# Optimization experiments

Hardware: AMD Instinct MI355X
Metric: run time of the kernel (lower is better)

Reference implementation:

```python
import jax, jax.numpy as jnp
import numpy as np

B, T, H = 1024, 128, 256
EPS = 1e-5


def _lstm(x, W_ih, W_hh, b_ih, b_hh):
    # x: [B,T,D] -> hs: [B,T,H], hn: [B,H]; PyTorch gate order i,f,g,o
    xp = jnp.einsum('btd,gd->btg', x, W_ih) + b_ih + b_hh  # [B,T,4H]
    h0 = jnp.zeros((x.shape[0], W_hh.shape[1]), x.dtype)

    def step(carry, xt):
        h, c = carry
        g = xt + h @ W_hh.T
        i, f, gg, o = jnp.split(g, 4, axis=-1)
        c = jax.nn.sigmoid(f) * c + jax.nn.sigmoid(i) * jnp.tanh(gg)
        h = jax.nn.sigmoid(o) * jnp.tanh(c)
        return (h, c), h

    (hn, _), hs = jax.lax.scan(step, (h0, h0), jnp.swapaxes(xp, 0, 1))
    return jnp.swapaxes(hs, 0, 1), hn


def _bn(x, g, b, m, v):
    # eval-mode BatchNorm1d
    return g * (x - m) * jax.lax.rsqrt(v + EPS) + b


def setup_inputs() -> dict:
    key = jax.random.key(0)
    ks = jax.random.split(key, 40)
    f = lambda i, shape, s=0.05: jax.random.normal(ks[i], shape, jnp.float32) * s
    d = {}
    d['seq_cont_data'] = f(0, (B, T, 64), 1.0)
    d['seq_cat_data'] = jax.random.randint(ks[1], (B, T, 2), 0, 500)
    d['non_seq_cat_data'] = jax.random.randint(ks[2], (B, 2), 0, 1000)
    d['non_seq_cont_data'] = f(3, (B, 32), 1.0)
    d['emb_ns0'] = f(4, (10000, 64))
    d['emb_ns1'] = f(5, (1000, 64))
    d['emb_s0'] = f(6, (1000, 32))
    d['emb_s1'] = f(7, (500, 32))
    d['W_ih'] = f(8, (4 * H, 128)); d['W_hh'] = f(9, (4 * H, H))
    d['b_ih'] = f(10, (4 * H,)); d['b_hh'] = f(11, (4 * H,))
    d['W_ltd'] = f(12, (H, H)); d['b_ltd'] = f(13, (H,))
    d['W_conv'] = f(14, (H, T)); d['b_conv'] = f(15, (H,))
    d['W_tpa'] = f(16, (H, H)); d['W_tpa_h'] = f(17, (H, H)); d['W_tpa_c'] = f(18, (H, H))
    FIN = 672
    d['W_f1'] = f(19, (512, FIN)); d['b_f1'] = f(20, (512,))
    d['g1'] = 1.0 + f(21, (512,)); d['be1'] = f(22, (512,)); d['m1'] = f(23, (512,)); d['v1'] = jnp.ones((512,), jnp.float32)
    d['W_f2'] = f(24, (256, 512)); d['b_f2'] = f(25, (256,))
    d['g2'] = 1.0 + f(26, (256,)); d['be2'] = f(27, (256,)); d['m2'] = f(28, (256,)); d['v2'] = jnp.ones((256,), jnp.float32)
    d['W_out'] = f(29, (64, 256)); d['b_out'] = f(30, (64,))
    return d


def reference(seq_cont_data, seq_cat_data, non_seq_cat_data, non_seq_cont_data,
              emb_ns0, emb_ns1, emb_s0, emb_s1,
              W_ih, W_hh, b_ih, b_hh, W_ltd, b_ltd, W_conv, b_conv,
              W_tpa, W_tpa_h, W_tpa_c,
              W_f1, b_f1, g1, be1, m1, v1,
              W_f2, b_f2, g2, be2, m2, v2,
              W_out, b_out):
    # non-sequential input: embeddings + continuous
    ns_cat = jnp.concatenate([emb_ns0[non_seq_cat_data[:, 0]], emb_ns1[non_seq_cat_data[:, 1]]], axis=1)
    non_seq_inp = jnp.concatenate([ns_cat, non_seq_cont_data], axis=1)  # [B,160]
    # sequential input: embeddings + continuous
    s_cat = jnp.concatenate([emb_s0[seq_cat_data[:, :, 0]], emb_s1[seq_cat_data[:, :, 1]]], axis=2)
    seq_data = jnp.concatenate([s_cat, seq_cont_data], axis=2)  # [B,T,128]
    output, hn = _lstm(seq_data, W_ih, W_hh, b_ih, b_hh)  # [B,T,H], [B,H]
    # TPA: hc[b,i,j] = Conv1d_j(output[:,:,i]) = sum_t output[b,t,i]*W_conv[j,t] + b_conv[j]
    hc = jnp.einsum('bti,jt->bij', output, W_conv) + b_conv  # [B,H,H]
    # alpha[b,i] = sigmoid( (hc[b,i] @ W_tpa.T) . hn[b] )
    alpha = jax.nn.sigmoid(jnp.einsum('bik,bk->bi', jnp.einsum('bij,kj->bik', hc, W_tpa), hn))
    vt = jnp.einsum('bi,bih->bh', alpha, hc)  # [B,H]
    htprime = hn @ W_tpa_h.T + vt @ W_tpa_c.T
    seq_inp = hn @ W_ltd.T + b_ltd
    fin_input = jnp.concatenate([non_seq_inp, seq_inp, htprime], axis=1)  # [B,672]
    x = _bn(jax.nn.relu(fin_input @ W_f1.T + b_f1), g1, be1, m1, v1)
    x = _bn(jax.nn.relu(x @ W_f2.T + b_f2), g2, be2, m2, v2)
    x = jax.nn.relu(x @ W_out.T + b_out)
    return x, fin_input
```

## Files before the change

kernel.cpp:

```cpp
#include <hip/hip_runtime.h>
#include <hip/hip_bf16.h>
#include <math.h>

#define B_SZ 1024
#define T_SZ 128
#define H_SZ 256
#define DIN  128
#define G4   1024
#define FINW 672

using bf16   = __hip_bfloat16;
using short8 = __attribute__((ext_vector_type(8))) short;
using f32x4  = __attribute__((ext_vector_type(4))) float;

__device__ __forceinline__ float bf2f(bf16 x) { return __bfloat162float(x); }
__device__ __forceinline__ bf16  f2bf(float x) { return __float2bfloat16(x); }
__device__ __forceinline__ float sigm(float x) { return 1.0f / (1.0f + __expf(-x)); }
__device__ __forceinline__ float ftanh(float x) { return 2.0f / (1.0f + __expf(-2.0f * x)) - 1.0f; }
__device__ __forceinline__ float bfraw2f(unsigned short r) {
  unsigned u = ((unsigned)r) << 16;
  return *reinterpret_cast<float*>(&u);
}

struct Ptrs { const void* p[33]; };

#define NSEG 30
__device__ __host__ constexpr int kSegOffArr(int i) {
  constexpr int off[NSEG + 1] = {
      0,       32768,   672768,  736768,  768768,  784768,  915840,
      1177984, 1179008, 1180032, 1245568, 1245824, 1278592, 1278848,
      1344384, 1409920, 1475456, 1819520, 1820032, 1820544, 1821056,
      1821568, 1822080, 1953152, 1953408, 1953664, 1953920, 1954176,
      1954432, 1970816, 1970880};
  return off[i];
}
#define ARENA_TOTAL 1970880
#define TR_BASE   1970880
#define TR_WthT   0
#define TR_WtcT   65536
#define TR_WltT   131072
#define TR_WcvT   196608
#define TR_TOTAL  229376
#define ARENA_TOTAL2 (ARENA_TOTAL + TR_TOTAL)

__global__ __launch_bounds__(256) void k_convert(Ptrs pk, bf16* __restrict__ dst,
                                                 uint4* __restrict__ hsp) {
  bool isf32 = ((((const unsigned*)pk.p[24])[0] & 0xFFFFu) == 0u);
  int stride = gridDim.x * blockDim.x;
  int gtid = blockIdx.x * blockDim.x + threadIdx.x;
  for (int i = gtid; i < ARENA_TOTAL; i += stride) {
    int s = 0, base = 0;
#pragma unroll
    for (int j = 1; j < NSEG; j++) {
      bool ge = (i >= kSegOffArr(j));
      s    = ge ? j : s;
      base = ge ? kSegOffArr(j) : base;
    }
    int off = i - base;
    const void* src = pk.p[3 + s];
    dst[i] = isf32 ? f2bf(((const float*)src)[off]) : ((const bf16*)src)[off];
  }
  for (int j = gtid; j < TR_TOTAL; j += stride) {
    const void* src;
    int off;
    if (j < TR_WtcT)      { src = pk.p[17]; int jj = j;            off = (jj & 255) * 256 + (jj >> 8); }
    else if (j < TR_WltT) { src = pk.p[18]; int jj = j - TR_WtcT;  off = (jj & 255) * 256 + (jj >> 8); }
    else if (j < TR_WcvT) { src = pk.p[12]; int jj = j - TR_WltT;  off = (jj & 255) * 256 + (jj >> 8); }
    else                  { src = pk.p[14]; int jj = j - TR_WcvT;  off = (jj & 255) * 128 + (jj >> 8); }
    dst[TR_BASE + j] = isf32 ? f2bf(((const float*)src)[off]) : ((const bf16*)src)[off];
  }
  uint4 pv = make_uint4(0xFFFFFFFFu, 0xFFFFFFFFu, 0xFFFFFFFFu, 0xFFFFFFFFu);
  for (int i = gtid; i < (int)((size_t)T_SZ * B_SZ * H_SZ * 2 / 16); i += stride)
    hsp[i] = pv;
}

__global__ __launch_bounds__(256) void k_gather(
    const void* __restrict__ seq_cont_raw, const int* __restrict__ seq_cat,
    const bf16* __restrict__ emb_s0, const bf16* __restrict__ emb_s1,
    bf16* __restrict__ seq_out, const unsigned* __restrict__ probe) {
  bool isf32 = ((probe[0] & 0xFFFFu) == 0u);
  int gid = blockIdx.x * blockDim.x + threadIdx.x;
  int seg = gid & 15;
  int m   = gid >> 4;
  int t   = m >> 10;
  int b   = m & 1023;
  bf16* dst = seq_out + (long)m * DIN + seg * 8;
  if (seg < 8) {
    const bf16* src;
    if (seg < 4) {
      int idx = seq_cat[(b * T_SZ + t) * 2 + 0];
      src = emb_s0 + idx * 32 + seg * 8;
    } else {
      int idx = seq_cat[(b * T_SZ + t) * 2 + 1];
      src = emb_s1 + idx * 32 + (seg - 4) * 8;
    }
    *reinterpret_cast<short8*>(dst) = *reinterpret_cast<const short8*>(src);
  } else {
    long base = ((long)b * T_SZ + t) * 64 + (seg - 8) * 8;
    if (isf32) {
      const float4* sp =
          reinterpret_cast<const float4*>((const float*)seq_cont_raw + base);
      float4 x0 = sp[0], x1 = sp[1];
      union { short8 v; bf16 h[8]; } u;
      u.h[0] = f2bf(x0.x); u.h[1] = f2bf(x0.y); u.h[2] = f2bf(x0.z); u.h[3] = f2bf(x0.w);
      u.h[4] = f2bf(x1.x); u.h[5] = f2bf(x1.y); u.h[6] = f2bf(x1.z); u.h[7] = f2bf(x1.w);
      *reinterpret_cast<short8*>(dst) = u.v;
    } else {
      *reinterpret_cast<short8*>(dst) =
          *reinterpret_cast<const short8*>((const bf16*)seq_cont_raw + base);
    }
  }
}

#define HPOISON 0xFFFFFFFFu
__global__ __launch_bounds__(512, 2) void k_lstm(
    const bf16* __restrict__ seq, const bf16* __restrict__ Wih,
    const bf16* __restrict__ Whh, const bf16* __restrict__ bih,
    const bf16* __restrict__ bhh, bf16* __restrict__ hs) {
  __shared__ short8 hsh[2][8 * 64];
  __shared__ short8 xsh[2][4 * 64];
  int tid  = threadIdx.x;
  int w    = tid >> 6, lane = tid & 63;
  int quad = lane >> 4, l15 = lane & 15;
  int bid  = blockIdx.x;
  int gid  = bid & 63;
  int rank = bid >> 6;
  int peer = 1 - rank;
  long b0  = (long)gid * 16;
  int hup = w * 16 + l15;
  int hu  = rank * 128 + hup;

  { short8 z = {0,0,0,0,0,0,0,0}; hsh[0][tid] = z; }

  float bia[4];
#pragma unroll
  for (int i = 0; i < 4; ++i) {
    int grow = i * H_SZ + hu;
    bia[i] = bf2f(bih[grow]) + bf2f(bhh[grow]);
  }

  short8 wif[4][4];
  short8 whfS[4][4];
  short8 whfP[4][4];
#pragma unroll
  for (int i = 0; i < 4; ++i) {
    long grow = (long)(i * H_SZ + rank * 128 + hup);
#pragma unroll
    for (int kt = 0; kt < 4; ++kt) {
      wif[i][kt] = *reinterpret_cast<const short8*>(
          Wih + grow * DIN + kt * 32 + quad * 8);
      whfS[i][kt] = *reinterpret_cast<const short8*>(
          Whh + grow * H_SZ + (rank * 4 + kt) * 32 + quad * 8);
      whfP[i][kt] = *reinterpret_cast<const short8*>(
          Whh + grow * H_SZ + (peer * 4 + kt) * 32 + quad * 8);
    }
  }
  if (tid < 256)
    xsh[0][tid] = *reinterpret_cast<const short8*>(
        seq + (b0 + (tid & 15)) * DIN + (tid >> 6) * 32 +
        ((tid >> 4) & 3) * 8);
  float c[4] = {0.f, 0.f, 0.f, 0.f};
  __syncthreads();

  for (int t = 0; t < T_SZ; ++t) {
    int cur = t & 1, nxt = cur ^ 1;
    short8 xpre;
    bool dopre = (t + 1 < T_SZ) & (tid < 256);
    if (dopre)
      xpre = *reinterpret_cast<const short8*>(
          seq + ((long)(t + 1) * B_SZ + b0 + (tid & 15)) * DIN +
          (tid >> 6) * 32 + ((tid >> 4) & 3) * 8);

    f32x4 acc[4];
#pragma unroll
    for (int i = 0; i < 4; ++i) acc[i] = {0.f, 0.f, 0.f, 0.f};

#pragma unroll
    for (int kt = 0; kt < 4; ++kt) {
      short8 ax = xsh[cur][kt * 64 + lane];
#pragma unroll
      for (int i = 0; i < 4; ++i)
        acc[i] = __builtin_amdgcn_mfma_f32_16x16x32_bf16(ax, wif[i][kt], acc[i], 0, 0, 0);
    }
#pragma unroll
    for (int kt = 0; kt < 4; ++kt) {
      short8 ah = hsh[cur][(rank * 4 + kt) * 64 + lane];
#pragma unroll
      for (int i = 0; i < 4; ++i)
        acc[i] = __builtin_amdgcn_mfma_f32_16x16x32_bf16(ah, whfS[i][kt], acc[i], 0, 0, 0);
    }

    if (t > 0) {
      if (tid < 256) {
        int m = tid >> 4, seg = tid & 15;
        const unsigned* src = reinterpret_cast<const unsigned*>(
            hs + ((long)(t - 1) * B_SZ + b0 + m) * H_SZ + peer * 128 + seg * 8);
        unsigned d0, d1, d2, d3;
        do {
          d0 = __hip_atomic_load(src + 0, __ATOMIC_RELAXED, __HIP_MEMORY_SCOPE_AGENT);
          d1 = __hip_atomic_load(src + 1, __ATOMIC_RELAXED, __HIP_MEMORY_SCOPE_AGENT);
          d2 = __hip_atomic_load(src + 2, __ATOMIC_RELAXED, __HIP_MEMORY_SCOPE_AGENT);
          d3 = __hip_atomic_load(src + 3, __ATOMIC_RELAXED, __HIP_MEMORY_SCOPE_AGENT);
        } while (d0 == HPOISON || d1 == HPOISON || d2 == HPOISON || d3 == HPOISON);
        union { unsigned u[4]; short8 s; } cv;
        cv.u[0] = d0; cv.u[1] = d1; cv.u[2] = d2; cv.u[3] = d3;
        hsh[cur][(peer * 4 + (seg >> 2)) * 64 + (seg & 3) * 16 + m] = cv.s;
      }
      __syncthreads();
    }
#pragma unroll
    for (int kt = 0; kt < 4; ++kt) {
      short8 ah = hsh[cur][(peer * 4 + kt) * 64 + lane];
#pragma unroll
      for (int i = 0; i < 4; ++i)
        acc[i] = __builtin_amdgcn_mfma_f32_16x16x32_bf16(ah, whfP[i][kt], acc[i], 0, 0, 0);
    }

    bf16* hbn = reinterpret_cast<bf16*>(&hsh[nxt][0]);
    unsigned hpk[4];
#pragma unroll
    for (int r = 0; r < 4; ++r) {
      float iv = sigm(acc[0][r] + bia[0]);
      float fv = sigm(acc[1][r] + bia[1]);
      float gv = ftanh(acc[2][r] + bia[2]);
      float ov = sigm(acc[3][r] + bia[3]);
      c[r] = fv * c[r] + iv * gv;
      bf16 hv = f2bf(ov * ftanh(c[r]));
      int m = quad * 4 + r;
      hbn[(((hu >> 5) * 64) + ((hu >> 3) & 3) * 16 + m) * 8 + (hu & 7)] = hv;
      unsigned hraw = (unsigned)*reinterpret_cast<unsigned short*>(&hv);
      unsigned nb = (unsigned)__shfl_down((int)hraw, 1, 64);
      hpk[r] = hraw | (nb << 16);
    }
    if (dopre) xsh[nxt][tid] = xpre;
    __syncthreads();
    if ((l15 & 1) == 0) {
#pragma unroll
      for (int r = 0; r < 4; ++r) {
        int m = quad * 4 + r;
        unsigned* dst = reinterpret_cast<unsigned*>(
            hs + ((long)t * B_SZ + b0 + m) * H_SZ + hu);
        __hip_atomic_store(dst, hpk[r], __ATOMIC_RELAXED,
                           __HIP_MEMORY_SCOPE_AGENT);
      }
    }
  }
}

__global__ __launch_bounds__(256) void k_u(
    const bf16* __restrict__ hs, const bf16* __restrict__ W_tpa,
    const bf16* __restrict__ W_conv, const bf16* __restrict__ b_conv,
    float* __restrict__ w2, float* __restrict__ c0) {
  __shared__ float hn_sh[8][256];
  __shared__ float u_sh[8][256];
  __shared__ float wred[4][8];
  int tid = threadIdx.x;
  long b0 = (long)blockIdx.x * 8;
#pragma unroll
  for (int r = 0; r < 8; r++)
    hn_sh[r][tid] = bf2f(hs[((long)(T_SZ - 1) * B_SZ + b0 + r) * H_SZ + tid]);
  __syncthreads();
  float u[8] = {0,0,0,0,0,0,0,0};
  for (int kk = 0; kk < 32; kk++) {
    float wv[8];
#pragma unroll
    for (int q = 0; q < 8; q++)
      wv[q] = bf2f(W_tpa[(kk * 8 + q) * H_SZ + tid]);
#pragma unroll
    for (int r = 0; r < 8; r++) {
      const float4* hp = reinterpret_cast<const float4*>(&hn_sh[r][kk * 8]);
      float4 h0 = hp[0], h1 = hp[1];
      u[r] += h0.x * wv[0]; u[r] += h0.y * wv[1];
      u[r] += h0.z * wv[2]; u[r] += h0.w * wv[3];
      u[r] += h1.x * wv[4]; u[r] += h1.y * wv[5];
      u[r] += h1.z * wv[6]; u[r] += h1.w * wv[7];
    }
  }
  float bc = bf2f(b_conv[tid]);
  float p[8];
#pragma unroll
  for (int r = 0; r < 8; r++) { u_sh[r][tid] = u[r]; p[r] = u[r] * bc; }
#pragma unroll
  for (int d = 32; d > 0; d >>= 1)
#pragma unroll
    for (int r = 0; r < 8; r++) p[r] += __shfl_down(p[r], d, 64);
  if ((tid & 63) == 0)
#pragma unroll
    for (int r = 0; r < 8; r++) wred[tid >> 6][r] = p[r];
  __syncthreads();
  if (tid < 8)
    c0[b0 + tid] = wred[0][tid] + wred[1][tid] + wred[2][tid] + wred[3][tid];
  if (tid < T_SZ) {
    float a[8] = {0,0,0,0,0,0,0,0};
    for (int jj = 0; jj < 32; jj++) {
      float wv[8];
#pragma unroll
      for (int q = 0; q < 8; q++)
        wv[q] = bf2f(W_conv[(jj * 8 + q) * T_SZ + tid]);
#pragma unroll
      for (int r = 0; r < 8; r++) {
        const float4* up = reinterpret_cast<const float4*>(&u_sh[r][jj * 8]);
        float4 u0 = up[0], u1 = up[1];
        a[r] += u0.x * wv[0]; a[r] += u0.y * wv[1];
        a[r] += u0.z * wv[2]; a[r] += u0.w * wv[3];
        a[r] += u1.x * wv[4]; a[r] += u1.y * wv[5];
        a[r] += u1.z * wv[6]; a[r] += u1.w * wv[7];
      }
    }
#pragma unroll
    for (int r = 0; r < 8; r++) w2[(b0 + r) * T_SZ + tid] = a[r];
  }
}

__global__ __launch_bounds__(256) void k_alphas(
    const bf16* __restrict__ hs, const float* __restrict__ w2,
    const float* __restrict__ c0, float* __restrict__ asum,
    float* __restrict__ sbuf) {
  __shared__ unsigned hc[128 * 129];
  __shared__ float w2s[T_SZ];
  __shared__ float ash[H_SZ];
  __shared__ float red[256];
  int b = blockIdx.x, tid = threadIdx.x;
#pragma unroll
  for (int p = 0; p < 16; p++) {
    int task = p * 256 + tid;
    int row = task >> 5, seg = task & 31;
    short8 v = *reinterpret_cast<const short8*>(
        hs + ((long)row * B_SZ + b) * H_SZ + seg * 8);
    union { short8 s; unsigned u[4]; } cv; cv.s = v;
#pragma unroll
    for (int k = 0; k < 4; k++) hc[row * 129 + seg * 4 + k] = cv.u[k];
  }
  if (tid < T_SZ) w2s[tid] = w2[b * T_SZ + tid];
  __syncthreads();
  {
    float ap = c0[b];
    int wi = tid >> 1, hi = tid & 1;
    for (int t = 0; t < T_SZ; t++) {
      unsigned uv = hc[t * 129 + wi];
      unsigned short h16 = hi ? (unsigned short)(uv >> 16) : (unsigned short)(uv & 0xFFFF);
      float hvf = __bfloat162float(*reinterpret_cast<bf16*>(&h16));
      ap += hvf * w2s[t];
    }
    float a = sigm(ap);
    ash[tid] = a;
    red[tid] = a;
  }
  __syncthreads();
  for (int s = 128; s > 0; s >>= 1) {
    if (tid < s) red[tid] += red[tid + s];
    __syncthreads();
  }
  if (tid == 0) asum[b] = red[0];
  if (tid < T_SZ) {
    float acc = 0.f;
    for (int k = 0; k < 128; k++) {
      int wi = (k + tid) & 127;
      unsigned uv = hc[tid * 129 + wi];
      unsigned short lo16 = (unsigned short)(uv & 0xFFFF);
      unsigned short hi16 = (unsigned short)(uv >> 16);
      float lo = __bfloat162float(*reinterpret_cast<bf16*>(&lo16));
      float hi = __bfloat162float(*reinterpret_cast<bf16*>(&hi16));
      acc += ash[2 * wi] * lo + ash[2 * wi + 1] * hi;
    }
    sbuf[b * T_SZ + tid] = acc;
  }
}

__global__ __launch_bounds__(256) void k_fin(
    const bf16* __restrict__ hs, const float* __restrict__ sbuf,
    const float* __restrict__ asum, const bf16* __restrict__ WcvT,
    const bf16* __restrict__ b_conv, const bf16* __restrict__ WthT,
    const bf16* __restrict__ WtcT, const bf16* __restrict__ WltT,
    const bf16* __restrict__ b_ltd, const int* __restrict__ ns_cat,
    const bf16* __restrict__ emb_ns0, const bf16* __restrict__ emb_ns1,
    const bf16* __restrict__ ns_cont, float* __restrict__ fin,
    void* __restrict__ d_out_raw, const unsigned* __restrict__ probe) {
  bool isf32 = ((probe[0] & 0xFFFFu) == 0u);
  __shared__ float s_sh[8][128];
  __shared__ float hn_sh[8][256];
  __shared__ float vt_sh[8][256];
  int tid = threadIdx.x;
  long b0 = (long)blockIdx.x * 8;
  auto store2 = [&](int r, int pos, float v) {
    fin[(b0 + r) * FINW + pos] = v;
    if (isf32)
      ((float*)d_out_raw + 65536)[(b0 + r) * FINW + pos] = v;
    else
      ((bf16*)d_out_raw + 65536)[(b0 + r) * FINW + pos] = f2bf(v);
  };
  if (tid < 128)
#pragma unroll
    for (int r = 0; r < 8; r++) s_sh[r][tid] = sbuf[(b0 + r) * T_SZ + tid];
#pragma unroll
  for (int r = 0; r < 8; r++)
    hn_sh[r][tid] = bf2f(hs[((long)(T_SZ - 1) * B_SZ + b0 + r) * H_SZ + tid]);
  __syncthreads();
  float vt[8] = {0,0,0,0,0,0,0,0};
  for (int tt = 0; tt < 16; tt++) {
    float wv[8];
#pragma unroll
    for (int q = 0; q < 8; q++)
      wv[q] = bf2f(WcvT[(tt * 8 + q) * H_SZ + tid]);
#pragma unroll
    for (int r = 0; r < 8; r++) {
      const float4* sp = reinterpret_cast<const float4*>(&s_sh[r][tt * 8]);
      float4 s0 = sp[0], s1 = sp[1];
      vt[r] += wv[0] * s0.x; vt[r] += wv[1] * s0.y;
      vt[r] += wv[2] * s0.z; vt[r] += wv[3] * s0.w;
      vt[r] += wv[4] * s1.x; vt[r] += wv[5] * s1.y;
      vt[r] += wv[6] * s1.z; vt[r] += wv[7] * s1.w;
    }
  }
  float bc = bf2f(b_conv[tid]);
#pragma unroll
  for (int r = 0; r < 8; r++) {
    vt[r] += bc * asum[b0 + r];
    vt_sh[r][tid] = vt[r];
  }
  __syncthreads();
  float htp[8] = {0,0,0,0,0,0,0,0}, sq[8] = {0,0,0,0,0,0,0,0};
  for (int kk = 0; kk < 32; kk++) {
    float wh[8], wc[8], wl[8];
#pragma unroll
    for (int q = 0; q < 8; q++) {
      int k = kk * 8 + q;
      wh[q] = bf2f(WthT[k * H_SZ + tid]);
      wc[q] = bf2f(WtcT[k * H_SZ + tid]);
      wl[q] = bf2f(WltT[k * H_SZ + tid]);
    }
#pragma unroll
    for (int r = 0; r < 8; r++) {
      const float4* hp = reinterpret_cast<const float4*>(&hn_sh[r][kk * 8]);
      const float4* vp = reinterpret_cast<const float4*>(&vt_sh[r][kk * 8]);
      float4 h0 = hp[0], h1 = hp[1], v0 = vp[0], v1 = vp[1];
      htp[r] += h0.x * wh[0] + v0.x * wc[0]; sq[r] += h0.x * wl[0];
      htp[r] += h0.y * wh[1] + v0.y * wc[1]; sq[r] += h0.y * wl[1];
      htp[r] += h0.z * wh[2] + v0.z * wc[2]; sq[r] += h0.z * wl[2];
      htp[r] += h0.w * wh[3] + v0.w * wc[3]; sq[r] += h0.w * wl[3];
      htp[r] += h1.x * wh[4] + v1.x * wc[4]; sq[r] += h1.x * wl[4];
      htp[r] += h1.y * wh[5] + v1.y * wc[5]; sq[r] += h1.y * wl[5];
      htp[r] += h1.z * wh[6] + v1.z * wc[6]; sq[r] += h1.z * wl[6];
      htp[r] += h1.w * wh[7] + v1.w * wc[7]; sq[r] += h1.w * wl[7];
    }
  }
  float bl = bf2f(b_ltd[tid]);
#pragma unroll
  for (int r = 0; r < 8; r++) {
    store2(r, 160 + tid, sq[r] + bl);
    store2(r, 416 + tid, htp[r]);
  }
  if (tid < 160) {
#pragma unroll
    for (int r = 0; r < 8; r++) {
      long b = b0 + r;
      float v;
      if (tid < 64)       v = bf2f(emb_ns0[(long)ns_cat[b * 2 + 0] * 64 + tid]);
      else if (tid < 128) v = bf2f(emb_ns1[(long)ns_cat[b * 2 + 1] * 64 + tid - 64]);
      else                v = bf2f(ns_cont[b * 32 + tid - 128]);
      store2(r, tid, v);
    }
  }
}

using short4v = __attribute__((ext_vector_type(4))) short;
__global__ __launch_bounds__(512) void k_mlp(
    const float* __restrict__ fin, const bf16* __restrict__ W_f1,
    const bf16* __restrict__ b_f1, const bf16* __restrict__ g1,
    const bf16* __restrict__ be1, const bf16* __restrict__ m1,
    const bf16* __restrict__ v1, const bf16* __restrict__ W_f2,
    const bf16* __restrict__ b_f2, const bf16* __restrict__ g2,
    const bf16* __restrict__ be2, const bf16* __restrict__ m2,
    const bf16* __restrict__ v2, const bf16* __restrict__ W_out,
    const bf16* __restrict__ b_out, void* __restrict__ d_out_raw,
    const unsigned* __restrict__ probe) {
  bool isf32 = ((probe[0] & 0xFFFFu) == 0u);
  __shared__ float a_sh[FINW * 8];
  __shared__ float x1t[512 * 8];
  __shared__ float x2t[256 * 8];
  int tid = threadIdx.x;
  long b0 = (long)blockIdx.x * 8;
  for (int i = tid; i < 8 * FINW; i += 512) {
    int r = i / FINW, k = i - r * FINW;
    a_sh[k * 8 + r] = fin[b0 * FINW + i];
  }
  __syncthreads();
  {
    int n = tid;
    float acc[8] = {0, 0, 0, 0, 0, 0, 0, 0};
    const short4v* wr4 = reinterpret_cast<const short4v*>(W_f1 + (long)n * FINW);
    for (int kk = 0; kk < FINW / 4; kk++) {
      short4v w4 = wr4[kk];
#pragma unroll
      for (int j = 0; j < 4; j++) {
        float wv = bfraw2f((unsigned short)w4[j]);
        const float4* ap = reinterpret_cast<const float4*>(&a_sh[(kk * 4 + j) * 8]);
        float4 a0 = ap[0], a1 = ap[1];
        acc[0] += wv * a0.x; acc[1] += wv * a0.y;
        acc[2] += wv * a0.z; acc[3] += wv * a0.w;
        acc[4] += wv * a1.x; acc[5] += wv * a1.y;
        acc[6] += wv * a1.z; acc[7] += wv * a1.w;
      }
    }
    float bb = bf2f(b_f1[n]);
    float scale = bf2f(g1[n]) * rsqrtf(bf2f(v1[n]) + 1e-5f);
    float mm = bf2f(m1[n]), bee = bf2f(be1[n]);
#pragma unroll
    for (int r = 0; r < 8; r++) {
      float x = acc[r] + bb;
      x = x > 0.f ? x : 0.f;
      x1t[n * 8 + r] = (x - mm) * scale + bee;
    }
  }
  __syncthreads();
  if (tid < 256) {
    int n = tid;
    float acc[8] = {0, 0, 0, 0, 0, 0, 0, 0};
    const short8* wr8 = reinterpret_cast<const short8*>(W_f2 + (long)n * 512);
    for (int kk = 0; kk < 64; kk++) {
      short8 w8 = wr8[kk];
#pragma unroll
      for (int j = 0; j < 8; j++) {
        float wv = bfraw2f((unsigned short)w8[j]);
        const float4* ap = reinterpret_cast<const float4*>(&x1t[(kk * 8 + j) * 8]);
        float4 a0 = ap[0], a1 = ap[1];
        acc[0] += wv * a0.x; acc[1] += wv * a0.y;
        acc[2] += wv * a0.z; acc[3] += wv * a0.w;
        acc[4] += wv * a1.x; acc[5] += wv * a1.y;
        acc[6] += wv * a1.z; acc[7] += wv * a1.w;
      }
    }
    float bb = bf2f(b_f2[n]);
    float scale = bf2f(g2[n]) * rsqrtf(bf2f(v2[n]) + 1e-5f);
    float mm = bf2f(m2[n]), bee = bf2f(be2[n]);
#pragma unroll
    for (int r = 0; r < 8; r++) {
      float x = acc[r] + bb;
      x = x > 0.f ? x : 0.f;
      x2t[n * 8 + r] = (x - mm) * scale + bee;
    }
  }
  __syncthreads();
  if (tid < 64) {
    int n = tid;
    float acc[8] = {0, 0, 0, 0, 0, 0, 0, 0};
    const short8* wr8 = reinterpret_cast<const short8*>(W_out + (long)n * H_SZ);
    for (int kk = 0; kk < 32; kk++) {
      short8 w8 = wr8[kk];
#pragma unroll
      for (int j = 0; j < 8; j++) {
        float wv = bfraw2f((unsigned short)w8[j]);
        const float4* ap = reinterpret_cast<const float4*>(&x2t[(kk * 8 + j) * 8]);
        float4 a0 = ap[0], a1 = ap[1];
        acc[0] += wv * a0.x; acc[1] += wv * a0.y;
        acc[2] += wv * a0.z; acc[3] += wv * a0.w;
        acc[4] += wv * a1.x; acc[5] += wv * a1.y;
        acc[6] += wv * a1.z; acc[7] += wv * a1.w;
      }
    }
    float bb = bf2f(b_out[n]);
#pragma unroll
    for (int r = 0; r < 8; r++) {
      float x = acc[r] + bb;
      x = x > 0.f ? x : 0.f;
      if (isf32)
        ((float*)d_out_raw)[(b0 + r) * 64 + n] = x;
      else
        ((bf16*)d_out_raw)[(b0 + r) * 64 + n] = f2bf(x);
    }
  }
}

extern "C" void kernel_launch(void* const* d_in, const int* in_sizes, int n_in,
                              void* d_out, int out_size, void* d_ws,
                              size_t ws_size, hipStream_t stream) {
  const int* seq_cat = (const int*)d_in[1];
  const int* ns_cat  = (const int*)d_in[2];
  const unsigned* probe = (const unsigned*)d_in[24];

  char* ws = (char*)d_ws;
  bf16* seqd  = (bf16*)ws;  ws += (size_t)T_SZ * B_SZ * DIN * 2;
  bf16* hsb   = (bf16*)ws;  ws += (size_t)T_SZ * B_SZ * H_SZ * 2;
  bf16* arena = (bf16*)ws;  ws += (size_t)ARENA_TOTAL2 * 2;
  float* w2   = (float*)ws; ws += (size_t)B_SZ * T_SZ * 4;
  float* c0   = (float*)ws; ws += (size_t)B_SZ * 4;
  float* asum = (float*)ws; ws += (size_t)B_SZ * 4;
  float* sbuf = (float*)ws; ws += (size_t)B_SZ * T_SZ * 4;
  float* fin  = (float*)ws; ws += (size_t)B_SZ * FINW * 4;

  const bf16* c_ns_cont = arena + 0;
  const bf16* c_emb_ns0 = arena + 32768;
  const bf16* c_emb_ns1 = arena + 672768;
  const bf16* c_emb_s0  = arena + 736768;
  const bf16* c_emb_s1  = arena + 768768;
  const bf16* c_W_ih    = arena + 784768;
  const bf16* c_W_hh    = arena + 915840;
  const bf16* c_b_ih    = arena + 1177984;
  const bf16* c_b_hh    = arena + 1179008;
  const bf16* c_b_ltd   = arena + 1245568;
  const bf16* c_b_conv  = arena + 1278592;
  const bf16* c_W_tpa   = arena + 1278848;
  const bf16* c_W_conv  = arena + 1245824;
  const bf16* c_W_f1    = arena + 1475456;
  const bf16* c_b_f1    = arena + 1819520;
  const bf16* c_g1      = arena + 1820032;
  const bf16* c_be1     = arena + 1820544;
  const bf16* c_m1      = arena + 1821056;
  const bf16* c_v1      = arena + 1821568;
  const bf16* c_W_f2    = arena + 1822080;
  const bf16* c_b_f2    = arena + 1953152;
  const bf16* c_g2      = arena + 1953408;
  const bf16* c_be2     = arena + 1953664;
  const bf16* c_m2      = arena + 1953920;
  const bf16* c_v2      = arena + 1954176;
  const bf16* c_W_out   = arena + 1954432;
  const bf16* c_b_out   = arena + 1970816;
  const bf16* c_WthT    = arena + TR_BASE + TR_WthT;
  const bf16* c_WtcT    = arena + TR_BASE + TR_WtcT;
  const bf16* c_WltT    = arena + TR_BASE + TR_WltT;
  const bf16* c_WcvT    = arena + TR_BASE + TR_WcvT;

  Ptrs pk;
  for (int i = 0; i < 33; i++) pk.p[i] = d_in[i];

  k_convert<<<dim3(512), 256, 0, stream>>>(pk, arena, (uint4*)hsb);
  k_gather<<<dim3(B_SZ * T_SZ * 16 / 256), 256, 0, stream>>>(
      d_in[0], seq_cat, c_emb_s0, c_emb_s1, seqd, probe);
  k_lstm<<<dim3(128), 512, 0, stream>>>(seqd, c_W_ih, c_W_hh, c_b_ih, c_b_hh,
                                        hsb);
  k_u<<<dim3(B_SZ / 8), 256, 0, stream>>>(hsb, c_W_tpa, c_W_conv, c_b_conv, w2, c0);
  k_alphas<<<dim3(B_SZ), 256, 0, stream>>>(hsb, w2, c0, asum, sbuf);
  k_fin<<<dim3(B_SZ / 8), 256, 0, stream>>>(hsb, sbuf, asum, c_WcvT, c_b_conv,
                                            c_WthT, c_WtcT, c_WltT,
                                            c_b_ltd, ns_cat, c_emb_ns0,
                                            c_emb_ns1, c_ns_cont, fin, d_out,
                                            probe);
  k_mlp<<<dim3(B_SZ / 8), 512, 0, stream>>>(fin, c_W_f1, c_b_f1, c_g1, c_be1,
                                            c_m1, c_v1, c_W_f2, c_b_f2, c_g2,
                                            c_be2, c_m2, c_v2, c_W_out, c_b_out,
                                            d_out, probe);
}
```

Baseline: 682.7 us.

## Fuse embedding gather into LSTM and merge fin/MLP kernels

Removes the separate gather kernel: the LSTM now builds each input fragment on the fly from the embedding tables and continuous data, so the staged seq buffer is neither written nor re-read. It also merges the fin and MLP kernels into one 512-thread kernel that keeps fin_input in shared memory instead of sending it through a global workspace. The trade-off is that the latency-bound LSTM prefetch now does dependent index loads plus fp32 conversion inside the recurrent loop, and the merged kernel uses more shared memory.

```diff
diff --git a/kernel.cpp b/kernel.cpp
--- a/kernel.cpp
+++ b/kernel.cpp
@@ -11,6 +11,7 @@
 
 using bf16   = __hip_bfloat16;
 using short8 = __attribute__((ext_vector_type(8))) short;
+using short4v = __attribute__((ext_vector_type(4))) short;
 using f32x4  = __attribute__((ext_vector_type(4))) float;
 
 __device__ __forceinline__ float bf2f(bf16 x) { return __bfloat162float(x); }
@@ -74,51 +75,43 @@
     hsp[i] = pv;
 }
 
-__global__ __launch_bounds__(256) void k_gather(
-    const void* __restrict__ seq_cont_raw, const int* __restrict__ seq_cat,
-    const bf16* __restrict__ emb_s0, const bf16* __restrict__ emb_s1,
-    bf16* __restrict__ seq_out, const unsigned* __restrict__ probe) {
-  bool isf32 = ((probe[0] & 0xFFFFu) == 0u);
-  int gid = blockIdx.x * blockDim.x + threadIdx.x;
-  int seg = gid & 15;
-  int m   = gid >> 4;
-  int t   = m >> 10;
-  int b   = m & 1023;
-  bf16* dst = seq_out + (long)m * DIN + seg * 8;
-  if (seg < 8) {
-    const bf16* src;
-    if (seg < 4) {
-      int idx = seq_cat[(b * T_SZ + t) * 2 + 0];
-      src = emb_s0 + idx * 32 + seg * 8;
-    } else {
-      int idx = seq_cat[(b * T_SZ + t) * 2 + 1];
-      src = emb_s1 + idx * 32 + (seg - 4) * 8;
-    }
-    *reinterpret_cast<short8*>(dst) = *reinterpret_cast<const short8*>(src);
+__device__ __forceinline__ short8 x_frag(
+    const void* __restrict__ cont_raw, bool isf32,
+    const int* __restrict__ seq_cat, const bf16* __restrict__ e0,
+    const bf16* __restrict__ e1, int b, int t, int kt, int qq) {
+  int f = kt * 32 + qq * 8;
+  if (kt == 0) {
+    int idx = seq_cat[(b * T_SZ + t) * 2 + 0];
+    return *reinterpret_cast<const short8*>(e0 + idx * 32 + f);
+  } else if (kt == 1) {
+    int idx = seq_cat[(b * T_SZ + t) * 2 + 1];
+    return *reinterpret_cast<const short8*>(e1 + idx * 32 + (f - 32));
   } else {
-    long base = ((long)b * T_SZ + t) * 64 + (seg - 8) * 8;
+    long base = ((long)b * T_SZ + t) * 64 + (f - 64);
     if (isf32) {
       const float4* sp =
-          reinterpret_cast<const float4*>((const float*)seq_cont_raw + base);
+          reinterpret_cast<const float4*>((const float*)cont_raw + base);
       float4 x0 = sp[0], x1 = sp[1];
       union { short8 v; bf16 h[8]; } u;
       u.h[0] = f2bf(x0.x); u.h[1] = f2bf(x0.y); u.h[2] = f2bf(x0.z); u.h[3] = f2bf(x0.w);
       u.h[4] = f2bf(x1.x); u.h[5] = f2bf(x1.y); u.h[6] = f2bf(x1.z); u.h[7] = f2bf(x1.w);
-      *reinterpret_cast<short8*>(dst) = u.v;
+      return u.v;
     } else {
-      *reinterpret_cast<short8*>(dst) =
-          *reinterpret_cast<const short8*>((const bf16*)seq_cont_raw + base);
+      return *reinterpret_cast<const short8*>((const bf16*)cont_raw + base);
     }
   }
 }
 
 #define HPOISON 0xFFFFFFFFu
 __global__ __launch_bounds__(512, 2) void k_lstm(
-    const bf16* __restrict__ seq, const bf16* __restrict__ Wih,
-    const bf16* __restrict__ Whh, const bf16* __restrict__ bih,
-    const bf16* __restrict__ bhh, bf16* __restrict__ hs) {
+    const void* __restrict__ cont_raw, const int* __restrict__ seq_cat,
+    const bf16* __restrict__ emb_s0, const bf16* __restrict__ emb_s1,
+    const bf16* __restrict__ Wih, const bf16* __restrict__ Whh,
+    const bf16* __restrict__ bih, const bf16* __restrict__ bhh,
+    bf16* __restrict__ hs, const unsigned* __restrict__ probe) {
   __shared__ short8 hsh[2][8 * 64];
   __shared__ short8 xsh[2][4 * 64];
+  bool isf32 = ((probe[0] & 0xFFFFu) == 0u);
   int tid  = threadIdx.x;
   int w    = tid >> 6, lane = tid & 63;
   int quad = lane >> 4, l15 = lane & 15;
@@ -129,6 +122,7 @@
   long b0  = (long)gid * 16;
   int hup = w * 16 + l15;
   int hu  = rank * 128 + hup;
+  int pm = tid & 15, pkt = tid >> 6, pqq = (tid >> 4) & 3;
 
   { short8 z = {0,0,0,0,0,0,0,0}; hsh[0][tid] = z; }
 
@@ -156,9 +150,8 @@
     }
   }
   if (tid < 256)
-    xsh[0][tid] = *reinterpret_cast<const short8*>(
-        seq + (b0 + (tid & 15)) * DIN + (tid >> 6) * 32 +
-        ((tid >> 4) & 3) * 8);
+    xsh[0][tid] = x_frag(cont_raw, isf32, seq_cat, emb_s0, emb_s1,
+                         (int)(b0 + pm), 0, pkt, pqq);
   float c[4] = {0.f, 0.f, 0.f, 0.f};
   __syncthreads();
 
@@ -167,9 +160,8 @@
     short8 xpre;
     bool dopre = (t + 1 < T_SZ) & (tid < 256);
     if (dopre)
-      xpre = *reinterpret_cast<const short8*>(
-          seq + ((long)(t + 1) * B_SZ + b0 + (tid & 15)) * DIN +
-          (tid >> 6) * 32 + ((tid >> 4) & 3) * 8);
+      xpre = x_frag(cont_raw, isf32, seq_cat, emb_s0, emb_s1,
+                    (int)(b0 + pm), t + 1, pkt, pqq);
 
     f32x4 acc[4];
 #pragma unroll
@@ -367,105 +359,14 @@
   }
 }
 
-__global__ __launch_bounds__(256) void k_fin(
+__global__ __launch_bounds__(512) void k_finmlp(
     const bf16* __restrict__ hs, const float* __restrict__ sbuf,
     const float* __restrict__ asum, const bf16* __restrict__ WcvT,
     const bf16* __restrict__ b_conv, const bf16* __restrict__ WthT,
     const bf16* __restrict__ WtcT, const bf16* __restrict__ WltT,
     const bf16* __restrict__ b_ltd, const int* __restrict__ ns_cat,
     const bf16* __restrict__ emb_ns0, const bf16* __restrict__ emb_ns1,
-    const bf16* __restrict__ ns_cont, float* __restrict__ fin,
-    void* __restrict__ d_out_raw, const unsigned* __restrict__ probe) {
-  bool isf32 = ((probe[0] & 0xFFFFu) == 0u);
-  __shared__ float s_sh[8][128];
-  __shared__ float hn_sh[8][256];
-  __shared__ float vt_sh[8][256];
-  int tid = threadIdx.x;
-  long b0 = (long)blockIdx.x * 8;
-  auto store2 = [&](int r, int pos, float v) {
-    fin[(b0 + r) * FINW + pos] = v;
-    if (isf32)
-      ((float*)d_out_raw + 65536)[(b0 + r) * FINW + pos] = v;
-    else
-      ((bf16*)d_out_raw + 65536)[(b0 + r) * FINW + pos] = f2bf(v);
-  };
-  if (tid < 128)
-#pragma unroll
-    for (int r = 0; r < 8; r++) s_sh[r][tid] = sbuf[(b0 + r) * T_SZ + tid];
-#pragma unroll
-  for (int r = 0; r < 8; r++)
-    hn_sh[r][tid] = bf2f(hs[((long)(T_SZ - 1) * B_SZ + b0 + r) * H_SZ + tid]);
-  __syncthreads();
-  float vt[8] = {0,0,0,0,0,0,0,0};
-  for (int tt = 0; tt < 16; tt++) {
-    float wv[8];
-#pragma unroll
-    for (int q = 0; q < 8; q++)
-      wv[q] = bf2f(WcvT[(tt * 8 + q) * H_SZ + tid]);
-#pragma unroll
-    for (int r = 0; r < 8; r++) {
-      const float4* sp = reinterpret_cast<const float4*>(&s_sh[r][tt * 8]);
-      float4 s0 = sp[0], s1 = sp[1];
-      vt[r] += wv[0] * s0.x; vt[r] += wv[1] * s0.y;
-      vt[r] += wv[2] * s0.z; vt[r] += wv[3] * s0.w;
-      vt[r] += wv[4] * s1.x; vt[r] += wv[5] * s1.y;
-      vt[r] += wv[6] * s1.z; vt[r] += wv[7] * s1.w;
-    }
-  }
-  float bc = bf2f(b_conv[tid]);
-#pragma unroll
-  for (int r = 0; r < 8; r++) {
-    vt[r] += bc * asum[b0 + r];
-    vt_sh[r][tid] = vt[r];
-  }
-  __syncthreads();
-  float htp[8] = {0,0,0,0,0,0,0,0}, sq[8] = {0,0,0,0,0,0,0,0};
-  for (int kk = 0; kk < 32; kk++) {
-    float wh[8], wc[8], wl[8];
-#pragma unroll
-    for (int q = 0; q < 8; q++) {
-      int k = kk * 8 + q;
-      wh[q] = bf2f(WthT[k * H_SZ + tid]);
-      wc[q] = bf2f(WtcT[k * H_SZ + tid]);
-      wl[q] = bf2f(WltT[k * H_SZ + tid]);
-    }
-#pragma unroll
-    for (int r = 0; r < 8; r++) {
-      const float4* hp = reinterpret_cast<const float4*>(&hn_sh[r][kk * 8]);
-      const float4* vp = reinterpret_cast<const float4*>(&vt_sh[r][kk * 8]);
-      float4 h0 = hp[0], h1 = hp[1], v0 = vp[0], v1 = vp[1];
-      htp[r] += h0.x * wh[0] + v0.x * wc[0]; sq[r] += h0.x * wl[0];
-      htp[r] += h0.y * wh[1] + v0.y * wc[1]; sq[r] += h0.y * wl[1];
-      htp[r] += h0.z * wh[2] + v0.z * wc[2]; sq[r] += h0.z * wl[2];
-      htp[r] += h0.w * wh[3] + v0.w * wc[3]; sq[r] += h0.w * wl[3];
-      htp[r] += h1.x * wh[4] + v1.x * wc[4]; sq[r] += h1.x * wl[4];
-      htp[r] += h1.y * wh[5] + v1.y * wc[5]; sq[r] += h1.y * wl[5];
-      htp[r] += h1.z * wh[6] + v1.z * wc[6]; sq[r] += h1.z * wl[6];
-      htp[r] += h1.w * wh[7] + v1.w * wc[7]; sq[r] += h1.w * wl[7];
-    }
-  }
-  float bl = bf2f(b_ltd[tid]);
-#pragma unroll
-  for (int r = 0; r < 8; r++) {
-    store2(r, 160 + tid, sq[r] + bl);
-    store2(r, 416 + tid, htp[r]);
-  }
-  if (tid < 160) {
-#pragma unroll
-    for (int r = 0; r < 8; r++) {
-      long b = b0 + r;
-      float v;
-      if (tid < 64)       v = bf2f(emb_ns0[(long)ns_cat[b * 2 + 0] * 64 + tid]);
-      else if (tid < 128) v = bf2f(emb_ns1[(long)ns_cat[b * 2 + 1] * 64 + tid - 64]);
-      else                v = bf2f(ns_cont[b * 32 + tid - 128]);
-      store2(r, tid, v);
-    }
-  }
-}
-
-using short4v = __attribute__((ext_vector_type(4))) short;
-__global__ __launch_bounds__(512) void k_mlp(
-    const float* __restrict__ fin, const bf16* __restrict__ W_f1,
+    const bf16* __restrict__ ns_cont, const bf16* __restrict__ W_f1,
     const bf16* __restrict__ b_f1, const bf16* __restrict__ g1,
     const bf16* __restrict__ be1, const bf16* __restrict__ m1,
     const bf16* __restrict__ v1, const bf16* __restrict__ W_f2,
@@ -475,14 +376,99 @@
     const bf16* __restrict__ b_out, void* __restrict__ d_out_raw,
     const unsigned* __restrict__ probe) {
   bool isf32 = ((probe[0] & 0xFFFFu) == 0u);
+  __shared__ float s_sh[8][128];
+  __shared__ float hn_sh[8][256];
+  __shared__ float vt_sh[8][256];
   __shared__ float a_sh[FINW * 8];
   __shared__ float x1t[512 * 8];
   __shared__ float x2t[256 * 8];
   int tid = threadIdx.x;
+  int h = tid & 255, rh = tid >> 8;
   long b0 = (long)blockIdx.x * 8;
-  for (int i = tid; i < 8 * FINW; i += 512) {
-    int r = i / FINW, k = i - r * FINW;
-    a_sh[k * 8 + r] = fin[b0 * FINW + i];
+  auto store2 = [&](int r, int pos, float v) {
+    a_sh[pos * 8 + r] = v;
+    if (isf32)
+      ((float*)d_out_raw + 65536)[(b0 + r) * FINW + pos] = v;
+    else
+      ((bf16*)d_out_raw + 65536)[(b0 + r) * FINW + pos] = f2bf(v);
+  };
+  if (tid < 128)
+#pragma unroll
+    for (int r = 0; r < 8; r++) s_sh[r][tid] = sbuf[(b0 + r) * T_SZ + tid];
+#pragma unroll
+  for (int rr = 0; rr < 4; rr++) {
+    int r = rh * 4 + rr;
+    hn_sh[r][h] = bf2f(hs[((long)(T_SZ - 1) * B_SZ + b0 + r) * H_SZ + h]);
+  }
+  __syncthreads();
+  float vt[4] = {0, 0, 0, 0};
+  for (int tt = 0; tt < 16; tt++) {
+    float wv[8];
+#pragma unroll
+    for (int q = 0; q < 8; q++)
+      wv[q] = bf2f(WcvT[(tt * 8 + q) * H_SZ + h]);
+#pragma unroll
+    for (int rr = 0; rr < 4; rr++) {
+      int r = rh * 4 + rr;
+      const float4* sp = reinterpret_cast<const float4*>(&s_sh[r][tt * 8]);
+      float4 s0 = sp[0], s1 = sp[1];
+      vt[rr] += wv[0] * s0.x; vt[rr] += wv[1] * s0.y;
+      vt[rr] += wv[2] * s0.z; vt[rr] += wv[3] * s0.w;
+      vt[rr] += wv[4] * s1.x; vt[rr] += wv[5] * s1.y;
+      vt[rr] += wv[6] * s1.z; vt[rr] += wv[7] * s1.w;
+    }
+  }
+  float bc = bf2f(b_conv[h]);
+#pragma unroll
+  for (int rr = 0; rr < 4; rr++) {
+    int r = rh * 4 + rr;
+    vt[rr] += bc * asum[b0 + r];
+    vt_sh[r][h] = vt[rr];
+  }
+  __syncthreads();
+  float htp[4] = {0, 0, 0, 0}, sq[4] = {0, 0, 0, 0};
+  for (int kk = 0; kk < 32; kk++) {
+    float wh[8], wc[8], wl[8];
+#pragma unroll
+    for (int q = 0; q < 8; q++) {
+      int k = kk * 8 + q;
+      wh[q] = bf2f(WthT[k * H_SZ + h]);
+      wc[q] = bf2f(WtcT[k * H_SZ + h]);
+      wl[q] = bf2f(WltT[k * H_SZ + h]);
+    }
+#pragma unroll
+    for (int rr = 0; rr < 4; rr++) {
+      int r = rh * 4 + rr;
+      const float4* hp = reinterpret_cast<const float4*>(&hn_sh[r][kk * 8]);
+      const float4* vp = reinterpret_cast<const float4*>(&vt_sh[r][kk * 8]);
+      float4 h0 = hp[0], h1 = hp[1], v0 = vp[0], v1 = vp[1];
+      htp[rr] += h0.x * wh[0] + v0.x * wc[0]; sq[rr] += h0.x * wl[0];
+      htp[rr] += h0.y * wh[1] + v0.y * wc[1]; sq[rr] += h0.y * wl[1];
+      htp[rr] += h0.z * wh[2] + v0.z * wc[2]; sq[rr] += h0.z * wl[2];
+      htp[rr] += h0.w * wh[3] + v0.w * wc[3]; sq[rr] += h0.w * wl[3];
+      htp[rr] += h1.x * wh[4] + v1.x * wc[4]; sq[rr] += h1.x * wl[4];
+      htp[rr] += h1.y * wh[5] + v1.y * wc[5]; sq[rr] += h1.y * wl[5];
+      htp[rr] += h1.z * wh[6] + v1.z * wc[6]; sq[rr] += h1.z * wl[6];
+      htp[rr] += h1.w * wh[7] + v1.w * wc[7]; sq[rr] += h1.w * wl[7];
+    }
+  }
+  float bl = bf2f(b_ltd[h]);
+#pragma unroll
+  for (int rr = 0; rr < 4; rr++) {
+    int r = rh * 4 + rr;
+    store2(r, 160 + h, sq[rr] + bl);
+    store2(r, 416 + h, htp[rr]);
+  }
+  if (tid < 160) {
+#pragma unroll
+    for (int r = 0; r < 8; r++) {
+      long b = b0 + r;
+      float v;
+      if (tid < 64)       v = bf2f(emb_ns0[(long)ns_cat[b * 2 + 0] * 64 + tid]);
+      else if (tid < 128) v = bf2f(emb_ns1[(long)ns_cat[b * 2 + 1] * 64 + tid - 64]);
+      else                v = bf2f(ns_cont[b * 32 + tid - 128]);
+      store2(r, tid, v);
+    }
   }
   __syncthreads();
   {
@@ -579,14 +565,12 @@
   const unsigned* probe = (const unsigned*)d_in[24];
 
   char* ws = (char*)d_ws;
-  bf16* seqd  = (bf16*)ws;  ws += (size_t)T_SZ * B_SZ * DIN * 2;
   bf16* hsb   = (bf16*)ws;  ws += (size_t)T_SZ * B_SZ * H_SZ * 2;
   bf16* arena = (bf16*)ws;  ws += (size_t)ARENA_TOTAL2 * 2;
   float* w2   = (float*)ws; ws += (size_t)B_SZ * T_SZ * 4;
   float* c0   = (float*)ws; ws += (size_t)B_SZ * 4;
   float* asum = (float*)ws; ws += (size_t)B_SZ * 4;
   float* sbuf = (float*)ws; ws += (size_t)B_SZ * T_SZ * 4;
-  float* fin  = (float*)ws; ws += (size_t)B_SZ * FINW * 4;
 
   const bf16* c_ns_cont = arena + 0;
   const bf16* c_emb_ns0 = arena + 32768;
@@ -598,9 +582,9 @@
   const bf16* c_b_ih    = arena + 1177984;
   const bf16* c_b_hh    = arena + 1179008;
   const bf16* c_b_ltd   = arena + 1245568;
+  const bf16* c_W_conv  = arena + 1245824;
   const bf16* c_b_conv  = arena + 1278592;
   const bf16* c_W_tpa   = arena + 1278848;
-  const bf16* c_W_conv  = arena + 1245824;
   const bf16* c_W_f1    = arena + 1475456;
   const bf16* c_b_f1    = arena + 1819520;
   const bf16* c_g1      = arena + 1820032;
@@ -624,19 +608,14 @@
   for (int i = 0; i < 33; i++) pk.p[i] = d_in[i];
 
   k_convert<<<dim3(512), 256, 0, stream>>>(pk, arena, (uint4*)hsb);
-  k_gather<<<dim3(B_SZ * T_SZ * 16 / 256), 256, 0, stream>>>(
-      d_in[0], seq_cat, c_emb_s0, c_emb_s1, seqd, probe);
-  k_lstm<<<dim3(128), 512, 0, stream>>>(seqd, c_W_ih, c_W_hh, c_b_ih, c_b_hh,
-                                        hsb);
+  k_lstm<<<dim3(128), 512, 0, stream>>>(d_in[0], seq_cat, c_emb_s0, c_emb_s1,
+                                        c_W_ih, c_W_hh, c_b_ih, c_b_hh, hsb,
+                                        probe);
   k_u<<<dim3(B_SZ / 8), 256, 0, stream>>>(hsb, c_W_tpa, c_W_conv, c_b_conv, w2, c0);
   k_alphas<<<dim3(B_SZ), 256, 0, stream>>>(hsb, w2, c0, asum, sbuf);
-  k_fin<<<dim3(B_SZ / 8), 256, 0, stream>>>(hsb, sbuf, asum, c_WcvT, c_b_conv,
-                                            c_WthT, c_WtcT, c_WltT,
-                                            c_b_ltd, ns_cat, c_emb_ns0,
-                                            c_emb_ns1, c_ns_cont, fin, d_out,
-                                            probe);
-  k_mlp<<<dim3(B_SZ / 8), 512, 0, stream>>>(fin, c_W_f1, c_b_f1, c_g1, c_be1,
-                                            c_m1, c_v1, c_W_f2, c_b_f2, c_g2,
-                                            c_be2, c_m2, c_v2, c_W_out, c_b_out,
-                                            d_out, probe);
-}
+  k_finmlp<<<dim3(B_SZ / 8), 512, 0, stream>>>(
+      hsb, sbuf, asum, c_WcvT, c_b_conv, c_WthT, c_WtcT, c_WltT, c_b_ltd,
+      ns_cat, c_emb_ns0, c_emb_ns1, c_ns_cont, c_W_f1, c_b_f1, c_g1, c_be1,
+      c_m1, c_v1, c_W_f2, c_b_f2, c_g2, c_be2, c_m2, c_v2, c_W_out, c_b_out,
+      d_out, probe);
+}
```

New measurement: 687.1 us. About the same (+0.6%).
